# Kernel tuning notes

Measured on AMD Instinct MI355X. Metric: run time of the kernel, lower is better.

Reference implementation:

```python
import jax, jax.numpy as jnp
import numpy as np
from jax import lax

M = 8   # num_heads
K = 4   # num_points


def conv2d(x, w, b, pad):
    # x: [B,C,H,W], w: [O,I,kh,kw]
    y = lax.conv_general_dilated(x, w, (1, 1), [(pad, pad), (pad, pad)],
                                 dimension_numbers=('NCHW', 'OIHW', 'NCHW'))
    return y + b[None, :, None, None]


def grid_sample_zeros(v, px, py):
    # Bilinear grid_sample, align_corners=True, padding_mode='zeros'.
    # v: [N,Cm,H,W]; px,py: [N,P] in pixel coordinates.
    N, Cm, H, W = v.shape
    x0 = jnp.floor(px); y0 = jnp.floor(py)
    x1 = x0 + 1.0;      y1 = y0 + 1.0
    wx = px - x0;       wy = py - y0
    vflat = v.reshape(N, Cm, H * W)

    def tap(xi, yi):
        valid = (xi >= 0) & (xi <= W - 1) & (yi >= 0) & (yi <= H - 1)
        xc = jnp.clip(xi, 0, W - 1).astype(jnp.int32)
        yc = jnp.clip(yi, 0, H - 1).astype(jnp.int32)
        idx = yc * W + xc                          # [N,P]
        g = jnp.take_along_axis(vflat, idx[:, None, :], axis=2)  # [N,Cm,P]
        return g * valid[:, None, :].astype(v.dtype)

    v00 = tap(x0, y0); v01 = tap(x1, y0)
    v10 = tap(x0, y1); v11 = tap(x1, y1)
    wx = wx[:, None, :]; wy = wy[:, None, :]
    return (v00 * (1 - wx) * (1 - wy) + v01 * wx * (1 - wy)
            + v10 * (1 - wx) * wy + v11 * wx * wy)


def setup_inputs() -> dict:
    key = jax.random.key(0)
    ks = jax.random.split(key, 16)
    B, C, H, W = 8, 256, 64, 64
    s = 0.02
    inp = {
        'f_recalib': jax.random.normal(ks[0], (B, C, H, W), jnp.float32),
        'f_orig':    jax.random.normal(ks[1], (B, C, H, W), jnp.float32),
        'offset_w': jax.random.normal(ks[2], (M * K * 2, C, 3, 3), jnp.float32) * s,
        'offset_b': jnp.zeros((M * K * 2,), jnp.float32),
        'attn_w':   jax.random.normal(ks[3], (M * K, C, 3, 3), jnp.float32) * s,
        'attn_b':   jnp.zeros((M * K,), jnp.float32),
        'value_w':  jax.random.normal(ks[4], (C, C, 1, 1), jnp.float32) * s,
        'value_b':  jnp.zeros((C,), jnp.float32),
        'proj_w':   jax.random.normal(ks[5], (C, C, 1, 1), jnp.float32) * s,
        'proj_b':   jnp.zeros((C,), jnp.float32),
        'mlp_w1':   jax.random.normal(ks[6], (2 * C, C, 1, 1), jnp.float32) * s,
        'mlp_b1':   jnp.zeros((2 * C,), jnp.float32),
        'mlp_w2':   jax.random.normal(ks[7], (C, 2 * C, 1, 1), jnp.float32) * s,
        'mlp_b2':   jnp.zeros((C,), jnp.float32),
    }
    return inp


def reference(f_recalib, f_orig, offset_w, offset_b, attn_w, attn_b,
              value_w, value_b, proj_w, proj_b,
              mlp_w1, mlp_b1, mlp_w2, mlp_b2):
    B, C, H, W = f_recalib.shape
    Cm = C // M

    offsets = conv2d(f_recalib, offset_w, offset_b, 1).reshape(B, M, K, 2, H, W)
    attn = conv2d(f_recalib, attn_w, attn_b, 1).reshape(B, M, K, H, W)
    attn = jax.nn.softmax(attn, axis=2)
    value = conv2d(f_recalib, value_w, value_b, 0)

    gy, gx = jnp.meshgrid(jnp.arange(H, dtype=jnp.float32),
                          jnp.arange(W, dtype=jnp.float32), indexing='ij')
    gx_sym = (W - 1) - gx  # horizontally mirrored x coordinate
    # pixel-space sampling locations (align_corners=True normalization is exactly
    # inverted by grid_sample's unnormalization, so work in pixel coords)
    px = gx_sym[None, None, None] + offsets[:, :, :, 0]  # [B,M,K,H,W]
    py = gy[None, None, None] + offsets[:, :, :, 1]

    v = value.reshape(B * M, Cm, H, W)
    sampled = grid_sample_zeros(v, px.reshape(B * M, -1), py.reshape(B * M, -1))
    sampled = sampled.reshape(B, M, Cm, K, H, W)

    out = (sampled * attn[:, :, None]).sum(axis=3).reshape(B, C, H, W)
    out = conv2d(out, proj_w, proj_b, 0) + f_orig
    h = jax.nn.relu(conv2d(out, mlp_w1, mlp_b1, 0))
    out = conv2d(h, mlp_w2, mlp_b2, 0) + out
    return out
```

## Files before the change

kernel.cpp:

```cpp
#include <hip/hip_runtime.h>
#include <cstddef>

#define P_ 4096
#define PW_ 66

using u16 = unsigned short;
typedef float  f32x4  __attribute__((ext_vector_type(4)));
typedef u16    u16x8  __attribute__((ext_vector_type(8)));
typedef u16    u16x4  __attribute__((ext_vector_type(4)));
typedef __bf16 bf16x8 __attribute__((ext_vector_type(8)));

#define DEVINL __device__ __forceinline__

DEVINL u16 f2bf(float f) {
    union { float f; unsigned u; } v; v.f = f;
    unsigned r = v.u + 0x7fffu + ((v.u >> 16) & 1u);
    return (u16)(r >> 16);
}
DEVINL float bf2f(u16 h) {
    union { unsigned u; float f; } v; v.u = ((unsigned)h) << 16;
    return v.f;
}

DEVINL f32x4 mfma16(u16x8 a, u16x8 b, f32x4 c) {
    return __builtin_amdgcn_mfma_f32_16x16x32_bf16(
        __builtin_bit_cast(bf16x8, a), __builtin_bit_cast(bf16x8, b), c, 0, 0, 0);
}

DEVINL void gload16(const u16* src, const u16* lds_dst) {
    __builtin_amdgcn_global_load_lds(
        (const __attribute__((address_space(1))) void*)src,
        (__attribute__((address_space(3))) void*)lds_dst, 16, 0, 0);
}

__global__ void prep_weights(const float* __restrict__ off_w, const float* __restrict__ attn_w,
                             const float* __restrict__ val_w, const float* __restrict__ proj_w,
                             const float* __restrict__ w1, const float* __restrict__ w2,
                             u16* __restrict__ wbf) {
    int idx = blockIdx.x * 256 + threadIdx.x;
    if (idx >= 614400) return;
    float v;
    if (idx < 221184) {
        int tap = idx / 24576, rem = idx - tap * 24576, oc = rem >> 8, ic = rem & 255;
        v = (oc < 64) ? off_w[(size_t)(oc * 256 + ic) * 9 + tap]
                      : attn_w[(size_t)((oc - 64) * 256 + ic) * 9 + tap];
    } else if (idx < 286720) v = val_w[idx - 221184];
    else if (idx < 352256)   v = proj_w[idx - 286720];
    else if (idx < 483328)   v = w1[idx - 352256];
    else                     v = w2[idx - 483328];
    wbf[idx] = f2bf(v);
}

__global__ __launch_bounds__(256) void to_nhwc_pad(const float* __restrict__ in,
                                                   u16* __restrict__ xp) {
    const int y = blockIdx.x, c0 = blockIdx.y * 64, b = blockIdx.z;
    __shared__ u16 ts[64 * 72];
    const int t = threadIdx.x, cl = t >> 4, xq = t & 15;

    if (y == 0) {
        const u16x8 z = (u16x8){0, 0, 0, 0, 0, 0, 0, 0};
        for (int q = t; q < 2080; q += 256) {
            const int p = q >> 3, c8 = q & 7;
            int row, col;
            if (p < 66)       { row = 0;  col = p; }
            else if (p < 132) { row = 65; col = p - 66; }
            else { const int q2 = p - 132; row = 1 + (q2 >> 1); col = (q2 & 1) * 65; }
            *(u16x8*)&xp[((size_t)(b * PW_ + row) * PW_ + col) * 256 + c0 + c8 * 8] = z;
        }
    }

    #pragma unroll
    for (int r = 0; r < 4; ++r) {
        const int c = r * 16 + cl;
        const float4 v = *(const float4*)&in[((size_t)(b * 256 + c0 + c)) * P_ + y * 64 + xq * 4];
        ts[(xq * 4 + 0) * 72 + c] = f2bf(v.x);
        ts[(xq * 4 + 1) * 72 + c] = f2bf(v.y);
        ts[(xq * 4 + 2) * 72 + c] = f2bf(v.z);
        ts[(xq * 4 + 3) * 72 + c] = f2bf(v.w);
    }
    __syncthreads();
    const int px = t >> 2, seg = t & 3;
    u16x8 o0, o1;
    #pragma unroll
    for (int j = 0; j < 8; ++j) {
        o0[j] = ts[px * 72 + seg * 16 + j];
        o1[j] = ts[px * 72 + seg * 16 + 8 + j];
    }
    const size_t base = ((size_t)(b * PW_ + y + 1) * PW_ + 1 + px) * 256 + c0 + seg * 16;
    *(u16x8*)&xp[base]     = o0;
    *(u16x8*)&xp[base + 8] = o1;
}

__global__ __launch_bounds__(256, 4) void conv3x3_mfma(
    const u16* __restrict__ xp, const u16* __restrict__ wconv,
    const float* __restrict__ off_b, const float* __restrict__ attn_b,
    u16* __restrict__ convout) {
    const int y = blockIdx.x, b = blockIdx.y;
    const int tid = threadIdx.x, w = tid >> 6, lane = tid & 63, g = lane >> 4, i = lane & 15;
    const int wm = w & 1, wn = w >> 1;
    const int srow = lane >> 4, sc = lane & 15;
    __shared__ u16 xs[64 * 128];
    __shared__ u16 wsL[96 * 128];

    f32x4 acc[2][3];
    #pragma unroll
    for (int mi = 0; mi < 2; ++mi)
        #pragma unroll
        for (int nj = 0; nj < 3; ++nj) acc[mi][nj] = (f32x4){0.f, 0.f, 0.f, 0.f};

    for (int tap = 0; tap < 9; ++tap) {
        const int dy = tap / 3, dx = tap % 3;
        const u16* xrow = xp + ((size_t)(b * PW_ + y + dy) * PW_ + dx) * 256;
        const u16* wt = wconv + (size_t)(tap * 96) * 256;
        for (int cc = 0; cc < 2; ++cc) {
            const int kc = cc * 128;
            #pragma unroll
            for (int t = 0; t < 4; ++t) {
                const int j = w * 4 + t;
                const int row = j * 4 + srow;
                const int cs = sc ^ (row & 7);
                gload16(xrow + (size_t)row * 256 + kc + (cs << 3), &xs[j * 512]);
            }
            #pragma unroll
            for (int t = 0; t < 6; ++t) {
                const int j = w * 6 + t;
                const int row = j * 4 + srow;
                const int cs = sc ^ (row & 7);
                gload16(wt + (size_t)row * 256 + kc + (cs << 3), &wsL[j * 512]);
            }
            __syncthreads();
            #pragma unroll
            for (int ks = 0; ks < 4; ++ks) {
                u16x8 a[2], bb[3];
                #pragma unroll
                for (int mi = 0; mi < 2; ++mi) {
                    const int pr = wm * 32 + mi * 16 + i;
                    a[mi] = *(const u16x8*)&xs[pr * 128 + (((ks * 4 + g) ^ (pr & 7)) << 3)];
                }
                #pragma unroll
                for (int nj = 0; nj < 3; ++nj) {
                    const int ocr = wn * 48 + nj * 16 + i;
                    bb[nj] = *(const u16x8*)&wsL[ocr * 128 + (((ks * 4 + g) ^ (ocr & 7)) << 3)];
                }
                #pragma unroll
                for (int mi = 0; mi < 2; ++mi)
                    #pragma unroll
                    for (int nj = 0; nj < 3; ++nj)
                        acc[mi][nj] = mfma16(a[mi], bb[nj], acc[mi][nj]);
            }
            __syncthreads();
        }
    }
    #pragma unroll
    for (int mi = 0; mi < 2; ++mi) {
        const int x0 = wm * 32 + mi * 16 + g * 4;
        #pragma unroll
        for (int nj = 0; nj < 3; ++nj) {
            const int oc = wn * 48 + nj * 16 + i;
            const float bv = (oc < 64) ? off_b[oc] : attn_b[oc - 64];
            #pragma unroll
            for (int r = 0; r < 4; ++r)
                convout[((size_t)(b * P_ + y * 64 + x0 + r)) * 96 + oc] =
                    f2bf(acc[mi][nj][r] + bv);
        }
    }
}

__global__ __launch_bounds__(256, 2) void gemm_dbuf(
    const u16* __restrict__ X, const u16* __restrict__ W,
    const float* __restrict__ bias, const void* __restrict__ resid,
    void* __restrict__ outA, u16* __restrict__ outB,
    const int KTOT, const int OC, const int mode, const int padded) {
    const int px0 = blockIdx.x * 128, oc0 = blockIdx.y * 128, b = blockIdx.z;
    const int tid = threadIdx.x, w = tid >> 6, lane = tid & 63, g = lane >> 4, i = lane & 15;
    const int wm = w & 1, wn = w >> 1;
    __shared__ u16 lds[32768];
    u16* xs = lds;
    u16* wsL = lds + 16384;

    const int srcC = (lane & 7) ^ ((lane >> 3) & 7);

    f32x4 acc[4][4];
    #pragma unroll
    for (int mi = 0; mi < 4; ++mi)
        #pragma unroll
        for (int nj = 0; nj < 4; ++nj) acc[mi][nj] = (f32x4){0.f, 0.f, 0.f, 0.f};

    const int NC = KTOT >> 6;

    auto stage = [&](int buf, int kc) {
        #pragma unroll
        for (int t = 0; t < 4; ++t) {
            const int j = w * 4 + t;
            const int row = j * 8 + (lane >> 3);
            const u16* sx;
            if (padded) {
                const int pxg = px0 + row;
                sx = X + ((size_t)(b * PW_ + (pxg >> 6) + 1) * PW_ + (pxg & 63) + 1) * 256
                       + kc + (srcC << 3);
            } else {
                sx = X + (size_t)(b * P_ + px0 + row) * KTOT + kc + (srcC << 3);
            }
            gload16(sx, &xs[buf * 8192 + j * 512]);
        }
        #pragma unroll
        for (int t = 0; t < 4; ++t) {
            const int j = w * 4 + t;
            const int row = j * 8 + (lane >> 3);
            gload16(W + (size_t)(oc0 + row) * KTOT + kc + (srcC << 3),
                    &wsL[buf * 8192 + j * 512]);
        }
    };

    stage(0, 0);
    stage(1, 64);
    asm volatile("s_waitcnt vmcnt(8)" ::: "memory");
    __builtin_amdgcn_s_barrier();

    for (int c = 0; c < NC; ++c) {
        const u16* xb = &xs[(c & 1) * 8192];
        const u16* wb = &wsL[(c & 1) * 8192];
        #pragma unroll
        for (int ks = 0; ks < 2; ++ks) {
            u16x8 a[4], bb[4];
            #pragma unroll
            for (int mi = 0; mi < 4; ++mi) {
                const int row = wm * 64 + mi * 16 + i;
                a[mi] = *(const u16x8*)&xb[row * 64 + (((ks * 4 + g) ^ (row & 7)) << 3)];
            }
            #pragma unroll
            for (int nj = 0; nj < 4; ++nj) {
                const int row = wn * 64 + nj * 16 + i;
                bb[nj] = *(const u16x8*)&wb[row * 64 + (((ks * 4 + g) ^ (row & 7)) << 3)];
            }
            #pragma unroll
            for (int mi = 0; mi < 4; ++mi)
                #pragma unroll
                for (int nj = 0; nj < 4; ++nj)
                    acc[mi][nj] = mfma16(a[mi], bb[nj], acc[mi][nj]);
        }
        __builtin_amdgcn_sched_barrier(0);
        __builtin_amdgcn_s_barrier();
        if (c + 2 < NC) {
            stage(c & 1, (c + 2) << 6);
            asm volatile("s_waitcnt vmcnt(8)" ::: "memory");
        } else {
            asm volatile("s_waitcnt vmcnt(0)" ::: "memory");
        }
        __builtin_amdgcn_s_barrier();
    }

    float* lf = (float*)lds;
    const int pxq = tid >> 2, segq = tid & 3;
    const int oclh = tid >> 1, shh = (tid & 1) * 32;

    #pragma unroll
    for (int h = 0; h < 2; ++h) {
        if (wm == h) {
            #pragma unroll
            for (int nj = 0; nj < 4; ++nj) {
                const int ocl = wn * 64 + nj * 16 + i;
                const float bv = bias[oc0 + ocl];
                #pragma unroll
                for (int mi = 0; mi < 4; ++mi)
                    #pragma unroll
                    for (int r = 0; r < 4; ++r)
                        lf[ocl * 66 + mi * 16 + g * 4 + r] = acc[mi][nj][r] + bv;
            }
        }
        __syncthreads();
        const int pxg0 = px0 + h * 64;

        if (mode == 4) {
            const float* rf = (const float*)resid;
            const size_t rb = ((size_t)b * 256 + oc0 + oclh) * P_ + pxg0 + shh;
            #pragma unroll
            for (int q = 0; q < 8; ++q) {
                const float4 r4 = *(const float4*)&rf[rb + q * 4];
                lf[oclh * 66 + shh + q * 4 + 0] += r4.x;
                lf[oclh * 66 + shh + q * 4 + 1] += r4.y;
                lf[oclh * 66 + shh + q * 4 + 2] += r4.z;
                lf[oclh * 66 + shh + q * 4 + 3] += r4.w;
            }
            __syncthreads();
        }

        if (mode <= 1 || mode == 4) {
            const size_t nb = ((size_t)(b * P_ + pxg0 + pxq)) * OC + oc0 + segq * 32;
            #pragma unroll
            for (int t2 = 0; t2 < 4; ++t2) {
                u16x8 o8;
                #pragma unroll
                for (int jj = 0; jj < 8; ++jj) {
                    float v = lf[(segq * 32 + t2 * 8 + jj) * 66 + pxq];
                    if (mode == 1) v = fmaxf(v, 0.f);
                    o8[jj] = f2bf(v);
                }
                *(u16x8*)&outB[nb + t2 * 8] = o8;
            }
        }
        if (mode == 4) {
            u16* on = (u16*)outA;
            const size_t cb = ((size_t)b * 256 + oc0 + oclh) * P_ + pxg0 + shh;
            #pragma unroll
            for (int t2 = 0; t2 < 4; ++t2) {
                u16x8 o8;
                #pragma unroll
                for (int jj = 0; jj < 8; ++jj)
                    o8[jj] = f2bf(lf[oclh * 66 + shh + t2 * 8 + jj]);
                *(u16x8*)&on[cb + t2 * 8] = o8;
            }
        }
        if (mode == 5) {
            const u16* rb16 = (const u16*)resid;
            float* of = (float*)outA;
            const size_t cb = ((size_t)b * 256 + oc0 + oclh) * P_ + pxg0 + shh;
            #pragma unroll
            for (int q = 0; q < 8; ++q) {
                const u16x4 r4 = *(const u16x4*)&rb16[cb + q * 4];
                float4 o;
                o.x = lf[oclh * 66 + shh + q * 4 + 0] + bf2f(r4[0]);
                o.y = lf[oclh * 66 + shh + q * 4 + 1] + bf2f(r4[1]);
                o.z = lf[oclh * 66 + shh + q * 4 + 2] + bf2f(r4[2]);
                o.w = lf[oclh * 66 + shh + q * 4 + 3] + bf2f(r4[3]);
                *(float4*)&of[cb + q * 4] = o;
            }
        }
        __syncthreads();
    }
}

__global__ __launch_bounds__(256) void sample_attend_bf(
    const u16* __restrict__ value, const u16* __restrict__ conv,
    u16* __restrict__ out1) {
    const int y = blockIdx.x, m = blockIdx.y, b = blockIdx.z;
    const int tid = threadIdx.x, x = tid >> 2, gq = tid & 3;
    const int w = tid >> 6, lane = tid & 63;
    const int wlo = max(0, y - 3), whi = min(63, y + 4);
    const int nchunks = (whi - wlo + 1) * 256;
    __shared__ u16 vlds[8 * 64 * 32];

    const u16* vbase = value + ((size_t)b * P_) * 256 + m * 32;
    for (int it = w; it * 64 < nchunks; it += 4) {
        const int cid = it * 64 + lane;
        const int r = cid >> 8, px = (cid >> 2) & 63, cc = cid & 3;
        gload16(vbase + ((size_t)((wlo + r) * 64 + px)) * 256 + cc * 8,
                &vlds[it * 512]);
    }

    const size_t prow = (size_t)(b * P_ + y * 64 + x);
    const u16x8 ov = *(const u16x8*)&conv[prow * 96 + m * 8];
    const u16x4 av = *(const u16x4*)&conv[prow * 96 + 64 + m * 4];
    float a[4];
    #pragma unroll
    for (int k = 0; k < 4; ++k) a[k] = bf2f(av[k]);
    const float mx = fmaxf(fmaxf(a[0], a[1]), fmaxf(a[2], a[3]));
    float s = 0.f;
    #pragma unroll
    for (int k = 0; k < 4; ++k) { a[k] = __expf(a[k] - mx); s += a[k]; }
    const float inv = 1.f / s;

    __syncthreads();

    float acc[8];
    #pragma unroll
    for (int j = 0; j < 8; ++j) acc[j] = 0.f;

    #pragma unroll
    for (int k = 0; k < 4; ++k) {
        const float offx = bf2f(ov[2 * k]), offy = bf2f(ov[2 * k + 1]);
        const float px = (float)(63 - x) + offx;
        const float py = (float)y + offy;
        const float x0f = floorf(px), y0f = floorf(py);
        const int xi0 = (int)x0f, yi0 = (int)y0f;
        const float wx = px - x0f, wy = py - y0f;
        const int xi1 = xi0 + 1, yi1 = yi0 + 1;
        const bool vx0 = (xi0 >= 0) & (xi0 <= 63), vx1 = (xi1 >= 0) & (xi1 <= 63);
        const bool vy0 = (yi0 >= 0) & (yi0 <= 63), vy1 = (yi1 >= 0) & (yi1 <= 63);
        const int cx0 = min(max(xi0, 0), 63), cx1 = min(max(xi1, 0), 63);
        const int cy0 = min(max(yi0, 0), 63), cy1 = min(max(yi1, 0), 63);
        const float ak = a[k] * inv;
        const float c00 = ak * (1.f - wx) * (1.f - wy) * ((vx0 & vy0) ? 1.f : 0.f);
        const float c01 = ak * wx * (1.f - wy) * ((vx1 & vy0) ? 1.f : 0.f);
        const float c10 = ak * (1.f - wx) * wy * ((vx0 & vy1) ? 1.f : 0.f);
        const float c11 = ak * wx * wy * ((vx1 & vy1) ? 1.f : 0.f);
        u16x8 v00, v01, v10, v11;
        const bool inWin = (cy0 >= wlo) & (cy1 <= whi);
        if (inWin) {
            const int r0 = (cy0 - wlo) * 64, r1 = (cy1 - wlo) * 64;
            v00 = *(const u16x8*)&vlds[(r0 + cx0) * 32 + gq * 8];
            v01 = *(const u16x8*)&vlds[(r0 + cx1) * 32 + gq * 8];
            v10 = *(const u16x8*)&vlds[(r1 + cx0) * 32 + gq * 8];
            v11 = *(const u16x8*)&vlds[(r1 + cx1) * 32 + gq * 8];
        } else {
            const u16* vb = vbase + gq * 8;
            v00 = *(const u16x8*)&vb[(size_t)(cy0 * 64 + cx0) * 256];
            v01 = *(const u16x8*)&vb[(size_t)(cy0 * 64 + cx1) * 256];
            v10 = *(const u16x8*)&vb[(size_t)(cy1 * 64 + cx0) * 256];
            v11 = *(const u16x8*)&vb[(size_t)(cy1 * 64 + cx1) * 256];
        }
        #pragma unroll
        for (int j = 0; j < 8; ++j)
            acc[j] += c00 * bf2f(v00[j]) + c01 * bf2f(v01[j])
                    + c10 * bf2f(v10[j]) + c11 * bf2f(v11[j]);
    }
    u16x8 o;
    #pragma unroll
    for (int j = 0; j < 8; ++j) o[j] = f2bf(acc[j]);
    *(u16x8*)&out1[prow * 256 + m * 32 + gq * 8] = o;
}

extern "C" void kernel_launch(void* const* d_in, const int* in_sizes, int n_in,
                              void* d_out, int out_size, void* d_ws, size_t ws_size,
                              hipStream_t stream) {
    const float* f_recalib = (const float*)d_in[0];
    const float* f_orig    = (const float*)d_in[1];
    const float* offset_w  = (const float*)d_in[2];
    const float* offset_b  = (const float*)d_in[3];
    const float* attn_w    = (const float*)d_in[4];
    const float* attn_b    = (const float*)d_in[5];
    const float* value_w   = (const float*)d_in[6];
    const float* value_b   = (const float*)d_in[7];
    const float* proj_w    = (const float*)d_in[8];
    const float* proj_b    = (const float*)d_in[9];
    const float* mlp_w1    = (const float*)d_in[10];
    const float* mlp_b1    = (const float*)d_in[11];
    const float* mlp_w2    = (const float*)d_in[12];
    const float* mlp_b2    = (const float*)d_in[13];
    float* out = (float*)d_out;

    u16* wsb       = (u16*)d_ws;
    u16* x_pad     = wsb;
    u16* convout   = wsb + 8921088;
    u16* value_bf  = wsb + 12066816;
    u16* out1_bf   = wsb + 20455424;
    u16* wbf       = wsb + 28844032;
    u16* out2_nchw = wsb + 29458432;
    u16* out2_bf   = x_pad;
    u16* h_bf      = wsb + 8921088;

    u16* wconv = wbf;
    u16* wval  = wbf + 221184;
    u16* wproj = wbf + 286720;
    u16* wmlp1 = wbf + 352256;
    u16* wmlp2 = wbf + 483328;

    prep_weights<<<2400, 256, 0, stream>>>(offset_w, attn_w, value_w, proj_w,
                                           mlp_w1, mlp_w2, wbf);
    to_nhwc_pad<<<dim3(64, 4, 8), 256, 0, stream>>>(f_recalib, x_pad);
    conv3x3_mfma<<<dim3(64, 8), 256, 0, stream>>>(x_pad, wconv, offset_b, attn_b, convout);
    gemm_dbuf<<<dim3(32, 2, 8), 256, 0, stream>>>(x_pad, wval, value_b, nullptr,
                                                  nullptr, value_bf, 256, 256, 0, 1);
    sample_attend_bf<<<dim3(64, 8, 8), 256, 0, stream>>>(value_bf, convout, out1_bf);
    gemm_dbuf<<<dim3(32, 2, 8), 256, 0, stream>>>(out1_bf, wproj, proj_b, f_orig,
                                                  out2_nchw, out2_bf, 256, 256, 4, 0);
    gemm_dbuf<<<dim3(32, 4, 8), 256, 0, stream>>>(out2_bf, wmlp1, mlp_b1, nullptr,
                                                  nullptr, h_bf, 256, 512, 1, 0);
    gemm_dbuf<<<dim3(32, 2, 8), 256, 0, stream>>>(h_bf, wmlp2, mlp_b2, out2_nchw,
                                                  out, nullptr, 512, 256, 5, 0);
}
```

Baseline: 150.2 us.

## Double-buffer conv3x3 LDS loads and merge weight prep into layout kernel

After: 143.7 us. 4.4% less time.

```diff
diff --git a/kernel.cpp b/kernel.cpp
--- a/kernel.cpp
+++ b/kernel.cpp
@@ -33,29 +33,34 @@
         (__attribute__((address_space(3))) void*)lds_dst, 16, 0, 0);
 }
 
-__global__ void prep_weights(const float* __restrict__ off_w, const float* __restrict__ attn_w,
-                             const float* __restrict__ val_w, const float* __restrict__ proj_w,
-                             const float* __restrict__ w1, const float* __restrict__ w2,
-                             u16* __restrict__ wbf) {
-    int idx = blockIdx.x * 256 + threadIdx.x;
-    if (idx >= 614400) return;
-    float v;
-    if (idx < 221184) {
-        int tap = idx / 24576, rem = idx - tap * 24576, oc = rem >> 8, ic = rem & 255;
-        v = (oc < 64) ? off_w[(size_t)(oc * 256 + ic) * 9 + tap]
-                      : attn_w[(size_t)((oc - 64) * 256 + ic) * 9 + tap];
-    } else if (idx < 286720) v = val_w[idx - 221184];
-    else if (idx < 352256)   v = proj_w[idx - 286720];
-    else if (idx < 483328)   v = w1[idx - 352256];
-    else                     v = w2[idx - 483328];
-    wbf[idx] = f2bf(v);
-}
-
-__global__ __launch_bounds__(256) void to_nhwc_pad(const float* __restrict__ in,
-                                                   u16* __restrict__ xp) {
-    const int y = blockIdx.x, c0 = blockIdx.y * 64, b = blockIdx.z;
+__global__ __launch_bounds__(256) void to_nhwc_pad(
+    const float* __restrict__ in, u16* __restrict__ xp,
+    const float* __restrict__ off_w, const float* __restrict__ attn_w,
+    const float* __restrict__ val_w, const float* __restrict__ proj_w,
+    const float* __restrict__ w1, const float* __restrict__ w2,
+    u16* __restrict__ wbf) {
+    const int bx = blockIdx.x, c0 = blockIdx.y * 64, b = blockIdx.z;
+    const int t = threadIdx.x;
+
+    if (bx >= 64) {
+        const int idx = ((bx - 64) * 32 + blockIdx.y * 8 + b) * 256 + t;
+        if (idx >= 614400) return;
+        float v;
+        if (idx < 221184) {
+            int tap = idx / 24576, rem = idx - tap * 24576, oc = rem >> 8, ic = rem & 255;
+            v = (oc < 64) ? off_w[(size_t)(oc * 256 + ic) * 9 + tap]
+                          : attn_w[(size_t)((oc - 64) * 256 + ic) * 9 + tap];
+        } else if (idx < 286720) v = val_w[idx - 221184];
+        else if (idx < 352256)   v = proj_w[idx - 286720];
+        else if (idx < 483328)   v = w1[idx - 352256];
+        else                     v = w2[idx - 483328];
+        wbf[idx] = f2bf(v);
+        return;
+    }
+
+    const int y = bx;
     __shared__ u16 ts[64 * 72];
-    const int t = threadIdx.x, cl = t >> 4, xq = t & 15;
+    const int cl = t >> 4, xq = t & 15;
 
     if (y == 0) {
         const u16x8 z = (u16x8){0, 0, 0, 0, 0, 0, 0, 0};
@@ -91,7 +96,7 @@
     *(u16x8*)&xp[base + 8] = o1;
 }
 
-__global__ __launch_bounds__(256, 4) void conv3x3_mfma(
+__global__ __launch_bounds__(256, 2) void conv3x3_mfma(
     const u16* __restrict__ xp, const u16* __restrict__ wconv,
     const float* __restrict__ off_b, const float* __restrict__ attn_b,
     u16* __restrict__ convout) {
@@ -99,8 +104,7 @@
     const int tid = threadIdx.x, w = tid >> 6, lane = tid & 63, g = lane >> 4, i = lane & 15;
     const int wm = w & 1, wn = w >> 1;
     const int srow = lane >> 4, sc = lane & 15;
-    __shared__ u16 xs[64 * 128];
-    __shared__ u16 wsL[96 * 128];
+    __shared__ u16 lds[40960];
 
     f32x4 acc[2][3];
     #pragma unroll
@@ -108,49 +112,67 @@
         #pragma unroll
         for (int nj = 0; nj < 3; ++nj) acc[mi][nj] = (f32x4){0.f, 0.f, 0.f, 0.f};
 
-    for (int tap = 0; tap < 9; ++tap) {
+    auto stage = [&](int buf, int c) {
+        const int tap = c >> 1, kc = (c & 1) * 128;
         const int dy = tap / 3, dx = tap % 3;
         const u16* xrow = xp + ((size_t)(b * PW_ + y + dy) * PW_ + dx) * 256;
         const u16* wt = wconv + (size_t)(tap * 96) * 256;
-        for (int cc = 0; cc < 2; ++cc) {
-            const int kc = cc * 128;
-            #pragma unroll
-            for (int t = 0; t < 4; ++t) {
-                const int j = w * 4 + t;
-                const int row = j * 4 + srow;
-                const int cs = sc ^ (row & 7);
-                gload16(xrow + (size_t)row * 256 + kc + (cs << 3), &xs[j * 512]);
-            }
-            #pragma unroll
-            for (int t = 0; t < 6; ++t) {
-                const int j = w * 6 + t;
-                const int row = j * 4 + srow;
-                const int cs = sc ^ (row & 7);
-                gload16(wt + (size_t)row * 256 + kc + (cs << 3), &wsL[j * 512]);
-            }
-            __syncthreads();
-            #pragma unroll
-            for (int ks = 0; ks < 4; ++ks) {
-                u16x8 a[2], bb[3];
+        u16* bufA = &lds[buf * 8192];
+        u16* bufW = &lds[16384 + buf * 12288];
+        #pragma unroll
+        for (int t = 0; t < 4; ++t) {
+            const int j = w * 4 + t;
+            const int row = j * 4 + srow;
+            const int cs = sc ^ (row & 7);
+            gload16(xrow + (size_t)row * 256 + kc + (cs << 3), &bufA[j * 512]);
+        }
+        #pragma unroll
+        for (int t = 0; t < 6; ++t) {
+            const int j = w * 6 + t;
+            const int row = j * 4 + srow;
+            const int cs = sc ^ (row & 7);
+            gload16(wt + (size_t)row * 256 + kc + (cs << 3), &bufW[j * 512]);
+        }
+    };
+
+    stage(0, 0);
+    stage(1, 1);
+    asm volatile("s_waitcnt vmcnt(10)" ::: "memory");
+    __builtin_amdgcn_s_barrier();
+
+    for (int c = 0; c < 18; ++c) {
+        const u16* bufA = &lds[(c & 1) * 8192];
+        const u16* bufW = &lds[16384 + (c & 1) * 12288];
+        #pragma unroll
+        for (int ks = 0; ks < 4; ++ks) {
+            u16x8 a[2], bb[3];
+            #pragma unroll
+            for (int mi = 0; mi < 2; ++mi) {
+                const int pr = wm * 32 + mi * 16 + i;
+                a[mi] = *(const u16x8*)&bufA[pr * 128 + (((ks * 4 + g) ^ (pr & 7)) << 3)];
+            }
+            #pragma unroll
+            for (int nj = 0; nj < 3; ++nj) {
+                const int ocr = wn * 48 + nj * 16 + i;
+                bb[nj] = *(const u16x8*)&bufW[ocr * 128 + (((ks * 4 + g) ^ (ocr & 7)) << 3)];
+            }
+            #pragma unroll
+            for (int mi = 0; mi < 2; ++mi)
                 #pragma unroll
-                for (int mi = 0; mi < 2; ++mi) {
-                    const int pr = wm * 32 + mi * 16 + i;
-                    a[mi] = *(const u16x8*)&xs[pr * 128 + (((ks * 4 + g) ^ (pr & 7)) << 3)];
-                }
-                #pragma unroll
-                for (int nj = 0; nj < 3; ++nj) {
-                    const int ocr = wn * 48 + nj * 16 + i;
-                    bb[nj] = *(const u16x8*)&wsL[ocr * 128 + (((ks * 4 + g) ^ (ocr & 7)) << 3)];
-                }
-                #pragma unroll
-                for (int mi = 0; mi < 2; ++mi)
-                    #pragma unroll
-                    for (int nj = 0; nj < 3; ++nj)
-                        acc[mi][nj] = mfma16(a[mi], bb[nj], acc[mi][nj]);
-            }
-            __syncthreads();
-        }
-    }
+                for (int nj = 0; nj < 3; ++nj)
+                    acc[mi][nj] = mfma16(a[mi], bb[nj], acc[mi][nj]);
+        }
+        __builtin_amdgcn_sched_barrier(0);
+        __builtin_amdgcn_s_barrier();
+        if (c + 2 < 18) {
+            stage(c & 1, c + 2);
+            asm volatile("s_waitcnt vmcnt(10)" ::: "memory");
+        } else {
+            asm volatile("s_waitcnt vmcnt(0)" ::: "memory");
+        }
+        __builtin_amdgcn_s_barrier();
+    }
+
     #pragma unroll
     for (int mi = 0; mi < 2; ++mi) {
         const int x0 = wm * 32 + mi * 16 + g * 4;
@@ -445,9 +467,8 @@
     u16* wmlp1 = wbf + 352256;
     u16* wmlp2 = wbf + 483328;
 
-    prep_weights<<<2400, 256, 0, stream>>>(offset_w, attn_w, value_w, proj_w,
-                                           mlp_w1, mlp_w2, wbf);
-    to_nhwc_pad<<<dim3(64, 4, 8), 256, 0, stream>>>(f_recalib, x_pad);
+    to_nhwc_pad<<<dim3(139, 4, 8), 256, 0, stream>>>(
+        f_recalib, x_pad, offset_w, attn_w, value_w, proj_w, mlp_w1, mlp_w2, wbf);
     conv3x3_mfma<<<dim3(64, 8), 256, 0, stream>>>(x_pad, wconv, offset_b, attn_b, convout);
     gemm_dbuf<<<dim3(32, 2, 8), 256, 0, stream>>>(x_pad, wval, value_b, nullptr,
                                                   nullptr, value_bf, 256, 256, 0, 1);
```
